# Performance work log

Measured on AMD Instinct MI355X. Metric: run time of the kernel, lower is better.

## Reference

```python
import jax, jax.numpy as jnp
import numpy as np

B, Qn, Kn, QD, KVD, FFN, H = 8, 1024, 2048, 512, 256, 2048, 8


def _layer_norm(x, g, b, eps=1e-5):
    m = jnp.mean(x, axis=-1, keepdims=True)
    v = jnp.mean((x - m) ** 2, axis=-1, keepdims=True)
    return (x - m) * jax.lax.rsqrt(v + eps) * g + b


def _mha(q, k, v, key_padding_mask, num_heads):
    # q,k: [B,S,D], v: [B,K,Dv]; reshape to per-head, scale by sqrt(key head dim)
    b, qn, d = q.shape
    kn = k.shape[1]
    dh = d // num_heads
    q = q.reshape(b, qn, num_heads, dh)
    k = k.reshape(b, kn, num_heads, dh)
    v = v.reshape(b, kn, num_heads, -1)
    attn = jnp.einsum('bqhd,bkhd->bhqk', q, k) / jnp.asarray(np.sqrt(dh), q.dtype)
    attn = jnp.where(key_padding_mask[:, None, None, :], -jnp.inf, attn)
    attn = jax.nn.softmax(attn, axis=-1)
    out = jnp.einsum('bhqk,bkhd->bqhd', attn, v)  # [B,Q,H,dv]
    return out.reshape(b, qn, -1)


def setup_inputs() -> dict:
    key = jax.random.key(0)
    ks = jax.random.split(key, 32)
    s = 0.02
    inp = {
        'queries_data': jax.random.normal(ks[0], (B, Qn, QD), jnp.float32),
        'queries_mask': jnp.zeros((B, Qn), bool),
        'box_pos': jax.random.normal(ks[1], (B, Qn, 4 * KVD), jnp.float32),
        'center_pos': jax.random.normal(ks[2], (B, Qn, 2 * KVD), jnp.float32),
        'kv_data': jax.random.normal(ks[3], (B, Kn, KVD), jnp.float32),
        'kv_mask': jnp.zeros((B, Kn), bool),
        'kv_pos': jax.random.normal(ks[4], (B, Kn, KVD), jnp.float32),
        # params ([in,out] convention)
        'sa_qkv_w': jax.random.normal(ks[5], (QD, 3 * QD), jnp.float32) * s,
        'sa_qkv_b': jnp.zeros((3 * QD,), jnp.float32),
        'sa_pos_w': jax.random.normal(ks[6], (4 * KVD, 2 * QD), jnp.float32) * s,
        'sa_pos_b': jnp.zeros((2 * QD,), jnp.float32),
        'sa_ln_g': jnp.ones((QD,), jnp.float32),
        'sa_ln_b': jnp.zeros((QD,), jnp.float32),
        'ca_q_w': jax.random.normal(ks[7], (QD, QD), jnp.float32) * s,
        'ca_q_b': jnp.zeros((QD,), jnp.float32),
        'ca_kv_w': jax.random.normal(ks[8], (KVD, 2 * QD), jnp.float32) * s,
        'ca_kv_b': jnp.zeros((2 * QD,), jnp.float32),
        'ca_qpos_w': jax.random.normal(ks[9], (2 * KVD, QD), jnp.float32) * s,
        'ca_qpos_b': jnp.zeros((QD,), jnp.float32),
        'ca_kpos_w': jax.random.normal(ks[10], (KVD, QD), jnp.float32) * s,
        'ca_kpos_b': jnp.zeros((QD,), jnp.float32),
        'ca_ln_g': jnp.ones((QD,), jnp.float32),
        'ca_ln_b': jnp.zeros((QD,), jnp.float32),
        'ffn_w1': jax.random.normal(ks[11], (QD, FFN), jnp.float32) * s,
        'ffn_b1': jnp.zeros((FFN,), jnp.float32),
        'ffn_w2': jax.random.normal(ks[12], (FFN, QD), jnp.float32) * s,
        'ffn_b2': jnp.zeros((QD,), jnp.float32),
        'ffn_ln_g': jnp.ones((QD,), jnp.float32),
        'ffn_ln_b': jnp.zeros((QD,), jnp.float32),
    }
    return inp


def reference(queries_data, queries_mask, box_pos, center_pos, kv_data, kv_mask, kv_pos,
              sa_qkv_w, sa_qkv_b, sa_pos_w, sa_pos_b, sa_ln_g, sa_ln_b,
              ca_q_w, ca_q_b, ca_kv_w, ca_kv_b, ca_qpos_w, ca_qpos_b,
              ca_kpos_w, ca_kpos_b, ca_ln_g, ca_ln_b,
              ffn_w1, ffn_b1, ffn_w2, ffn_b2, ffn_ln_g, ffn_ln_b):
    # ---- self-attention (pos added to q,k) ----
    qkv = queries_data @ sa_qkv_w + sa_qkv_b
    q, k, v = jnp.split(qkv, 3, axis=-1)
    q_pos, k_pos = jnp.split(box_pos @ sa_pos_w + sa_pos_b, 2, axis=-1)
    sa_out = _mha(q + q_pos, k + k_pos, v, queries_mask, H)
    sa_out = _layer_norm(queries_data + sa_out, sa_ln_g, sa_ln_b)
    # ---- cross-attention (pos concatenated per head) ----
    q = sa_out @ ca_q_w + ca_q_b
    k, v = jnp.split(kv_data @ ca_kv_w + ca_kv_b, 2, axis=-1)
    q_pos = center_pos @ ca_qpos_w + ca_qpos_b
    k_pos = kv_pos @ ca_kpos_w + ca_kpos_b
    dh = QD // H
    q = jnp.concatenate([q.reshape(B, Qn, H, dh), q_pos.reshape(B, Qn, H, dh)], axis=-1).reshape(B, Qn, -1)
    k = jnp.concatenate([k.reshape(B, Kn, H, dh), k_pos.reshape(B, Kn, H, dh)], axis=-1).reshape(B, Kn, -1)
    ca_out = _mha(q, k, v, kv_mask, H)
    ca_out = _layer_norm(sa_out + ca_out, ca_ln_g, ca_ln_b)
    # ---- FFN ----
    f = jax.nn.relu(ca_out @ ffn_w1 + ffn_b1) @ ffn_w2 + ffn_b2
    return _layer_norm(ca_out + f, ffn_ln_g, ffn_ln_b)
```

## Files before the change

kernel.cpp:

```cpp
#include <hip/hip_runtime.h>

typedef __attribute__((ext_vector_type(4))) float f32x4;
typedef __attribute__((ext_vector_type(8))) short bf16x8;
typedef __attribute__((ext_vector_type(4))) unsigned int u32x4;

static __device__ __forceinline__ short f2bf(float f){
    unsigned int u = __builtin_bit_cast(unsigned int, f);
    unsigned int r = (u + 0x7fffu + ((u >> 16) & 1u)) >> 16;
    return (short)r;
}
static __device__ __forceinline__ void gload_lds16(const void* g, void* l){
    __builtin_amdgcn_global_load_lds((const __attribute__((address_space(1))) void*)g,
                                     (__attribute__((address_space(3))) void*)l, 16, 0, 0);
}
static __device__ __forceinline__ float exp2fast(float x){
    float r; asm("v_exp_f32 %0, %1" : "=v"(r) : "v"(x)); return r;
}
static __device__ __forceinline__ unsigned int packbf(float lo, float hi){
#if __has_builtin(__builtin_amdgcn_perm)
    return __builtin_amdgcn_perm(__builtin_bit_cast(unsigned int, hi),
                                 __builtin_bit_cast(unsigned int, lo), 0x07060302u);
#else
    return (__builtin_bit_cast(unsigned int, hi) & 0xffff0000u) |
           (__builtin_bit_cast(unsigned int, lo) >> 16);
#endif
}
static __device__ __forceinline__ void prio_hi(){
#if defined(__HIP_DEVICE_COMPILE__)
    __builtin_amdgcn_s_setprio(1);
#endif
}
static __device__ __forceinline__ void prio_lo(){
#if defined(__HIP_DEVICE_COMPILE__)
    __builtin_amdgcn_s_setprio(0);
#endif
}

static __device__ __forceinline__ void transcast_body(const float* __restrict__ w,
                                                      short* __restrict__ wT,
                                                      int K, int N, int bx, int by, int t){
    int n = bx * 256 + t;
    int k0 = by * 8;
    bf16x8 o;
#pragma unroll
    for (int j = 0; j < 8; j++) o[j] = f2bf(w[(long)(k0 + j) * N + n]);
    *(bf16x8*)(wT + (long)n * K + k0) = o;
}
__global__ __launch_bounds__(256) void prep_weights(
    const float* __restrict__ queries, const float* __restrict__ box,
    const float* __restrict__ ctr, const float* __restrict__ kvd, const float* __restrict__ kvp,
    const unsigned char* __restrict__ qmask, const unsigned char* __restrict__ kmask,
    const float* __restrict__ b_qkv, const float* __restrict__ b_pos,
    short* __restrict__ Xcat, short* __restrict__ ctr_bf,
    short* __restrict__ kvd_bf, short* __restrict__ kvp_bf,
    float* __restrict__ mb_sa, float* __restrict__ mb_ca, float* __restrict__ bcomb,
    const float* __restrict__ w_qkv, const float* __restrict__ w_pos,
    const float* __restrict__ w_caq, const float* __restrict__ w_cakv,
    const float* __restrict__ w_caqp, const float* __restrict__ w_cakp,
    const float* __restrict__ w_f1, const float* __restrict__ w_f2,
    short* __restrict__ wTm_qk, short* __restrict__ wTv,
    short* __restrict__ wT_caq, short* __restrict__ wT_cakv,
    short* __restrict__ wT_caqp, short* __restrict__ wT_cakp,
    short* __restrict__ wT_f1, short* __restrict__ wT_f2)
{
    int bb = blockIdx.x, t = threadIdx.x;
    if (bb < 12288){
        const float* src; short* dst; long i; long stride; int logRow; int colOff;
        if (bb < 2048){ src = queries; dst = Xcat; i = ((long)bb * 256 + t) * 8; logRow = 9;  stride = 1536; colOff = 0; }
        else if (bb < 6144){ src = box; dst = Xcat; i = ((long)(bb - 2048) * 256 + t) * 8; logRow = 10; stride = 1536; colOff = 512; }
        else if (bb < 8192){ src = ctr; dst = ctr_bf; i = ((long)(bb - 6144) * 256 + t) * 8; logRow = 0; stride = 0; colOff = 0; }
        else if (bb < 10240){ src = kvd; dst = kvd_bf; i = ((long)(bb - 8192) * 256 + t) * 8; logRow = 0; stride = 0; colOff = 0; }
        else { src = kvp; dst = kvp_bf; i = ((long)(bb - 10240) * 256 + t) * 8; logRow = 0; stride = 0; colOff = 0; }
        f32x4 a = *(const f32x4*)(src + i);
        f32x4 b = *(const f32x4*)(src + i + 4);
        bf16x8 o;
#pragma unroll
        for (int j = 0; j < 4; j++){ o[j] = f2bf(a[j]); o[4 + j] = f2bf(b[j]); }
        long oi = logRow ? ((i >> logRow) * stride + colOff + (i & ((1L << logRow) - 1))) : i;
        *(bf16x8*)(dst + oi) = o;
        return;
    }
    if (bb < 12320){ int i = (bb - 12288) * 256 + t; mb_sa[i] = qmask[i] ? -1e30f : 0.f; return; }
    if (bb < 12384){ int i = (bb - 12320) * 256 + t; mb_ca[i] = kmask[i] ? -1e30f : 0.f; return; }
    if (bb < 12388){ int i = (bb - 12384) * 256 + t; if (i < 1024) bcomb[i] = b_qkv[i] + b_pos[i]; return; }
    int wb = bb - 12388;
    if (wb < 768){
        int by = wb / 4, bx = wb % 4;
        int n = bx * 256 + t;
        int k0 = by * 8;
        bf16x8 o;
#pragma unroll
        for (int j = 0; j < 8; j++){
            int kk = k0 + j;
            float v = (kk < 512) ? w_qkv[(long)kk * 1536 + n] : w_pos[(long)(kk - 512) * 1024 + n];
            o[j] = f2bf(v);
        }
        *(bf16x8*)(wTm_qk + (long)n * 1536 + k0) = o;
    }
    else if (wb < 896){
        int lb = wb - 768;
        int by = lb / 2, bx = lb % 2;
        int n = bx * 256 + t;
        int k0 = by * 8;
        bf16x8 o;
#pragma unroll
        for (int j = 0; j < 8; j++) o[j] = f2bf(w_qkv[(long)(k0 + j) * 1536 + 1024 + n]);
        *(bf16x8*)(wTv + (long)n * 512 + k0) = o;
    }
    else if (wb < 1024){ int lb = wb - 896;  transcast_body(w_caq,  wT_caq,  512, 512,  lb % 2, lb / 2, t); }
    else if (wb < 1152){ int lb = wb - 1024; transcast_body(w_cakv, wT_cakv, 256, 1024, lb % 4, lb / 4, t); }
    else if (wb < 1280){ int lb = wb - 1152; transcast_body(w_caqp, wT_caqp, 512, 512,  lb % 2, lb / 2, t); }
    else if (wb < 1344){ int lb = wb - 1280; transcast_body(w_cakp, wT_cakp, 256, 512,  lb % 2, lb / 2, t); }
    else if (wb < 1856){ int lb = wb - 1344; transcast_body(w_f1,   wT_f1,   512, 2048, lb % 8, lb / 8, t); }
    else               { int lb = wb - 1856; transcast_body(w_f2,   wT_f2,   2048, 512, lb % 2, lb / 2, t); }
}

struct GD {
    const short* A; const short* Bt; const float* bias;
    short* Cbf; float* Cf; short* Vt;
    long lda;
    int N, K, flags, vtColBase, snShift, vtSN, blkStart, nbx, nblk;
};
struct GD4 { GD g[4]; int n; };

__global__ __launch_bounds__(128, 3) void gemm_multi(GD4 dd)
{
    constexpr int BN = 64, BLOCK = 128;
    constexpr int BUF = (128 + BN) * 32;
    constexpr int EST = BN + 4;
    __shared__ __attribute__((aligned(16))) char smem[2 * BUF * 2];
    float* lC = (float*)smem;
    int bb = blockIdx.x;
    int si = 0;
#pragma unroll
    for (int i = 1; i < 4; i++) if (i < dd.n && bb >= dd.g[i].blkStart) si = i;
    const short* A = dd.g[si].A;
    const short* Bt = dd.g[si].Bt;
    const float* bias = dd.g[si].bias;
    short* Cbf = dd.g[si].Cbf;
    float* Cf = dd.g[si].Cf;
    short* Vt = dd.g[si].Vt;
    long lda = dd.g[si].lda;
    int N = dd.g[si].N, K = dd.g[si].K, flags = dd.g[si].flags;
    int vtColBase = dd.g[si].vtColBase, snShift = dd.g[si].snShift, vtSN = dd.g[si].vtSN;
    int nbx = dd.g[si].nbx, nblk = dd.g[si].nblk;

    int t = threadIdx.x, w = t >> 6, l = t & 63;
    int cl = l & 15, g = l >> 4;
    int flat = bb - dd.g[si].blkStart;
    int q8 = nblk >> 3;
    int swz = (flat & 7) * q8 + (flat >> 3);
    long r0 = (long)(swz / nbx) * 128, c0 = (long)(swz % nbx) * BN;
    int wr = w;
    f32x4 acc[4][4];
#pragma unroll
    for (int mi = 0; mi < 4; mi++)
#pragma unroll
        for (int ni = 0; ni < 4; ni++) acc[mi][ni] = f32x4{0.f, 0.f, 0.f, 0.f};

    auto stage = [&](int d, int k0){
        char* lA = smem + (size_t)d * BUF * 2;
        char* lB = lA + 128 * 32 * 2;
#pragma unroll
        for (int i = 0; i < 4; i++){
            int s = i * BLOCK + t;
            int row = s >> 2, blk = s & 3;
            int sb = blk ^ (row & 3);
            gload_lds16(A + (r0 + row) * lda + k0 + sb * 8, lA + i * (BLOCK * 16) + w * 1024);
        }
#pragma unroll
        for (int i = 0; i < 2; i++){
            int s = i * BLOCK + t;
            int row = s >> 2, blk = s & 3;
            int sb = blk ^ (row & 3);
            gload_lds16(Bt + (c0 + row) * (long)K + k0 + sb * 8, lB + i * (BLOCK * 16) + w * 1024);
        }
    };

    stage(0, 0);
    __syncthreads();
    int NK = K / 32;
    for (int kt = 0; kt < NK; kt++){
        int cur = kt & 1;
        if (kt + 1 < NK) stage(cur ^ 1, (kt + 1) * 32);
        const short* lA = (const short*)(smem + (size_t)cur * BUF * 2);
        const short* lB = lA + 128 * 32;
        bf16x8 af[4], bfr[4];
#pragma unroll
        for (int mi = 0; mi < 4; mi++){
            int row = wr * 64 + mi * 16 + cl;
            af[mi] = *(const bf16x8*)(lA + row * 32 + (g ^ (row & 3)) * 8);
        }
#pragma unroll
        for (int ni = 0; ni < 4; ni++){
            int row = ni * 16 + cl;
            bfr[ni] = *(const bf16x8*)(lB + row * 32 + (g ^ (row & 3)) * 8);
        }
        prio_hi();
#pragma unroll
        for (int mi = 0; mi < 4; mi++)
#pragma unroll
            for (int ni = 0; ni < 4; ni++)
                acc[mi][ni] = __builtin_amdgcn_mfma_f32_16x16x32_bf16(af[mi], bfr[ni], acc[mi][ni], 0, 0, 0);
        prio_lo();
        __syncthreads();
    }

    bool vtBlock = (flags & 4) && (c0 >= vtColBase);
#pragma unroll
    for (int mi = 0; mi < 4; mi++){
        __syncthreads();
#pragma unroll
        for (int ni = 0; ni < 4; ni++)
#pragma unroll
            for (int rr = 0; rr < 4; rr++)
                lC[(wr * 16 + g * 4 + rr) * EST + ni * 16 + cl] = acc[mi][ni][rr];
        __syncthreads();
        if (vtBlock){
#pragma unroll
            for (int c2 = 0; c2 < 2; c2++){
                int task = t + BLOCK * c2;
                int col = task & 63;
                int wrg = (task >> 6) & 1;
                int ch = task >> 7;
                float bv = bias[c0 + col];
                long qg0 = r0 + wrg * 64 + mi * 16 + ch * 8;
                bf16x8 ob;
#pragma unroll
                for (int j = 0; j < 8; j++)
                    ob[j] = f2bf(lC[(wrg * 16 + ch * 8 + j) * EST + col] + bv);
                long dvg = c0 - vtColBase + col;
                long h = dvg >> 6, dvv = dvg & 63;
                long b = qg0 >> snShift;
                long loc = qg0 & ((1L << snShift) - 1);
                *(bf16x8*)(Vt + ((b * 8 + h) * 64 + dvv) * (long)vtSN + loc) = ob;
            }
        } else {
#pragma unroll
            for (int c2 = 0; c2 < 2; c2++){
                int chunk = t + BLOCK * c2;
                int row = chunk >> 3;
                int coloff = (chunk & 7) * 8;
                long grow = r0 + (row >> 4) * 64 + mi * 16 + (row & 15);
                long gcol = c0 + coloff;
                f32x4 bv0 = *(const f32x4*)(bias + gcol);
                f32x4 bv1 = *(const f32x4*)(bias + gcol + 4);
                float v[8];
#pragma unroll
                for (int j = 0; j < 8; j++){
                    float x = lC[row * EST + coloff + j] + (j < 4 ? bv0[j] : bv1[j - 4]);
                    if (flags & 1) x = fmaxf(x, 0.f);
                    v[j] = x;
                }
                if (Cf){
                    *(f32x4*)(Cf + grow * N + gcol) = f32x4{v[0], v[1], v[2], v[3]};
                    *(f32x4*)(Cf + grow * N + gcol + 4) = f32x4{v[4], v[5], v[6], v[7]};
                } else {
                    bf16x8 ob;
#pragma unroll
                    for (int j = 0; j < 8; j++) ob[j] = f2bf(v[j]);
                    long idx;
                    if (flags & 2){
                        long part = gcol >> 9;
                        long cc = gcol & 511;
                        long b = grow >> 10, qn = grow & 1023;
                        long h = cc >> 6, d = cc & 63;
                        idx = ((part * 64 + b * 8 + h) * 1024 + qn) * 64 + d;
                    } else if (flags & 4){
                        idx = grow * (long)vtColBase + gcol;
                    } else {
                        idx = grow * N + gcol;
                    }
                    *(bf16x8*)(Cbf + idx) = ob;
                }
            }
        }
    }
}

__global__ __launch_bounds__(256) void ln_fuse(const float* __restrict__ a, const float* __restrict__ b,
                                               const float* __restrict__ g, const float* __restrict__ be,
                                               float* __restrict__ outf, short* __restrict__ outb){
    int w = threadIdx.x >> 6, l = threadIdx.x & 63;
    long row = (long)blockIdx.x * 4 + w;
    long base = row * 512 + l * 8;
    f32x4 a0 = *(const f32x4*)(a + base);
    f32x4 a1 = *(const f32x4*)(a + base + 4);
    f32x4 b0 = *(const f32x4*)(b + base);
    f32x4 b1 = *(const f32x4*)(b + base + 4);
    float x[8]; float s = 0.f, s2 = 0.f;
#pragma unroll
    for (int j = 0; j < 4; j++){ x[j] = a0[j] + b0[j]; x[4 + j] = a1[j] + b1[j]; }
#pragma unroll
    for (int j = 0; j < 8; j++){ s += x[j]; s2 += x[j] * x[j]; }
#pragma unroll
    for (int o = 1; o < 64; o <<= 1){ s += __shfl_xor(s, o); s2 += __shfl_xor(s2, o); }
    float mean = s * (1.f / 512.f);
    float rstd = rsqrtf(s2 * (1.f / 512.f) - mean * mean + 1e-5f);
    int c = l * 8;
    f32x4 y0, y1; bf16x8 ob;
#pragma unroll
    for (int j = 0; j < 4; j++){
        float y = (x[j] - mean) * rstd * g[c + j] + be[c + j];
        y0[j] = y; ob[j] = f2bf(y);
    }
#pragma unroll
    for (int j = 0; j < 4; j++){
        float y = (x[4 + j] - mean) * rstd * g[c + 4 + j] + be[c + 4 + j];
        y1[j] = y; ob[4 + j] = f2bf(y);
    }
    *(f32x4*)(outf + base) = y0;
    *(f32x4*)(outf + base + 4) = y1;
    if (outb) *(bf16x8*)(outb + base) = ob;
}

template<int DH, int KN, bool CAT>
__global__ __launch_bounds__(256, 2) void attn_kernel(
    const short* __restrict__ Q1, const short* __restrict__ Q2,
    const short* __restrict__ K1, const short* __restrict__ K2,
    const short* __restrict__ Vt,
    const float* __restrict__ mbias, float* __restrict__ out, float scale2)
{
    constexpr int KT = 64, DV = 64, Qn = 1024, H = 8;
    constexpr int NF = DH / 32;
    constexpr int BPR = DH / 8;
    constexpr int KITER = KT * BPR / 256;
    constexpr int NT = KN / KT;
    __shared__ __attribute__((aligned(16))) short lK[2][KT * DH];
    __shared__ __attribute__((aligned(16))) short lV[2][DV * KT];
    int t = threadIdx.x, w = t >> 6, l = t & 63;
    int cl = l & 15, g = l >> 4;
    int bid = blockIdx.x;
    int bh = (bid & 7) * 8 + (bid >> 6);
    int qb = (bid >> 3) & 7;
    int b = bh >> 3, h = bh & 7;
    int q0 = qb * 128 + w * 32;

    bf16x8 qf[2][NF];
#pragma unroll
    for (int qq = 0; qq < 2; qq++)
#pragma unroll
        for (int f = 0; f < NF; f++){
            if constexpr (CAT){
                const short* src = (f < NF / 2) ? Q1 : Q2;
                qf[qq][f] = *(const bf16x8*)(src + ((long)b * Qn + q0 + qq * 16 + cl) * 512 + h * 64
                                             + (f & (NF / 2 - 1)) * 32 + 8 * g);
            } else {
                qf[qq][f] = *(const bf16x8*)(Q1 + ((long)bh * Qn + q0 + qq * 16 + cl) * DH + f * 32 + 8 * g);
            }
        }

    const short* kp[KITER];
    long kstep[KITER];
#pragma unroll
    for (int i = 0; i < KITER; i++){
        int s_ = i * 256 + t;
        int srow_ = s_ / BPR, blk = s_ % BPR;
        int s32 = srow_ & 31;
        int key = (srow_ & 32) + 8 * ((s32 >> 2) & 3) + 4 * (s32 >> 4) + (s32 & 3);
        int sb = blk ^ (srow_ & 7);
        if constexpr (CAT){
            if (sb < 8){ kp[i] = K1 + ((long)b * KN + key) * 512 + h * 64 + sb * 8; kstep[i] = (long)KT * 512; }
            else       { kp[i] = K2 + ((long)b * KN + key) * 512 + h * 64 + (sb - 8) * 8; kstep[i] = (long)KT * 512; }
        } else {
            kp[i] = K1 + ((long)bh * KN + key) * DH + sb * 8; kstep[i] = (long)KT * DH;
        }
    }
    const short* vp[2];
#pragma unroll
    for (int i = 0; i < 2; i++){
        int s_ = i * 256 + t;
        int srow_ = s_ >> 3, blk = s_ & 7;
        int sb = blk ^ (srow_ & 7);
        vp[i] = Vt + ((long)bh * DV + srow_) * KN + sb * 8;
    }

    auto stage = [&](int d){
#pragma unroll
        for (int i = 0; i < KITER; i++){
            gload_lds16(kp[i], (char*)(&lK[d][0]) + i * 4096 + w * 1024);
            kp[i] += kstep[i];
        }
#pragma unroll
        for (int i = 0; i < 2; i++){
            gload_lds16(vp[i], (char*)(&lV[d][0]) + i * 4096 + w * 1024);
            vp[i] += KT;
        }
    };

    f32x4 st[2][4];
    auto do_qk = [&](int d){
        prio_hi();
#pragma unroll
        for (int o = 0; o < 4; o++){
            int srow_ = o * 16 + cl;
            bf16x8 kf[NF];
#pragma unroll
            for (int f = 0; f < NF; f++){
                int sb = (4 * f + g) ^ (srow_ & 7);
                kf[f] = *(const bf16x8*)(&lK[d][0] + srow_ * DH + sb * 8);
            }
#pragma unroll
            for (int qq = 0; qq < 2; qq++){
                f32x4 acc = f32x4{0.f, 0.f, 0.f, 0.f};
#pragma unroll
                for (int f = 0; f < NF; f++)
                    acc = __builtin_amdgcn_mfma_f32_16x16x32_bf16(kf[f], qf[qq][f], acc, 0, 0, 0);
                st[qq][o] = acc;
            }
        }
        prio_lo();
    };

    const float* mrow = mbias + (long)b * KN;
    bf16x8 vones;
    {
        u32x4 ou; ou[0] = ou[1] = ou[2] = ou[3] = 0x3F803F80u;
        vones = __builtin_bit_cast(bf16x8, ou);
    }
    f32x4 lacc[2];
    f32x4 oacc[2][4];
#pragma unroll
    for (int qq = 0; qq < 2; qq++){
        lacc[qq] = f32x4{0.f, 0.f, 0.f, 0.f};
#pragma unroll
        for (int d = 0; d < 4; d++) oacc[qq][d] = f32x4{0.f, 0.f, 0.f, 0.f};
    }

    f32x4 mb[4];
#pragma unroll
    for (int o = 0; o < 4; o++)
        mb[o] = *(const f32x4*)(mrow + (o >> 1) * 32 + 8 * g + 4 * (o & 1));

    stage(0);
    __syncthreads();
    do_qk(0);

    for (int tt = 0; tt < NT; tt++){
        int cur = tt & 1;
        if (tt + 1 < NT) stage(cur ^ 1);

        bf16x8 pa[2][2];
#pragma unroll
        for (int qq = 0; qq < 2; qq++){
#pragma unroll
            for (int kb = 0; kb < 2; kb++){
                float pA[4], pB[4];
#pragma unroll
                for (int rr = 0; rr < 4; rr++){
                    pA[rr] = exp2fast(fmaf(st[qq][2 * kb][rr], scale2, mb[2 * kb][rr]));
                    pB[rr] = exp2fast(fmaf(st[qq][2 * kb + 1][rr], scale2, mb[2 * kb + 1][rr]));
                }
                u32x4 pk;
                pk[0] = packbf(pA[0], pA[1]);
                pk[1] = packbf(pA[2], pA[3]);
                pk[2] = packbf(pB[0], pB[1]);
                pk[3] = packbf(pB[2], pB[3]);
                pa[qq][kb] = __builtin_bit_cast(bf16x8, pk);
            }
        }
        if (tt + 1 < NT){
#pragma unroll
            for (int o = 0; o < 4; o++)
                mb[o] = *(const f32x4*)(mrow + (tt + 1) * KT + (o >> 1) * 32 + 8 * g + 4 * (o & 1));
        }
        prio_hi();
#pragma unroll
        for (int qq = 0; qq < 2; qq++){
            lacc[qq] = __builtin_amdgcn_mfma_f32_16x16x32_bf16(pa[qq][0], vones, lacc[qq], 0, 0, 0);
            lacc[qq] = __builtin_amdgcn_mfma_f32_16x16x32_bf16(pa[qq][1], vones, lacc[qq], 0, 0, 0);
        }
#pragma unroll
        for (int dvc = 0; dvc < 4; dvc++){
            int vrow = dvc * 16 + cl;
            bf16x8 vf[2];
#pragma unroll
            for (int kb = 0; kb < 2; kb++){
                int sb = (4 * kb + g) ^ (vrow & 7);
                vf[kb] = *(const bf16x8*)(&lV[cur][0] + vrow * KT + sb * 8);
            }
#pragma unroll
            for (int qq = 0; qq < 2; qq++){
                f32x4 o = oacc[qq][dvc];
                o = __builtin_amdgcn_mfma_f32_16x16x32_bf16(pa[qq][0], vf[0], o, 0, 0, 0);
                o = __builtin_amdgcn_mfma_f32_16x16x32_bf16(pa[qq][1], vf[1], o, 0, 0, 0);
                oacc[qq][dvc] = o;
            }
        }
        prio_lo();
        __syncthreads();
        if (tt + 1 < NT) do_qk(cur ^ 1);
    }

#pragma unroll
    for (int qq = 0; qq < 2; qq++){
        float linv[4];
#pragma unroll
        for (int rr = 0; rr < 4; rr++) linv[rr] = 1.f / lacc[qq][rr];
#pragma unroll
        for (int dvc = 0; dvc < 4; dvc++)
#pragma unroll
            for (int rr = 0; rr < 4; rr++){
                int q = q0 + qq * 16 + 4 * g + rr;
                out[(((long)b * Qn + q) * H + h) * DV + dvc * 16 + cl] = oacc[qq][dvc][rr] * linv[rr];
            }
    }
}

extern "C" void kernel_launch(void* const* d_in, const int* in_sizes, int n_in,
                              void* d_out, int out_size, void* d_ws, size_t ws_size,
                              hipStream_t stream)
{
    (void)in_sizes; (void)n_in; (void)out_size; (void)ws_size;
    const int Qn = 1024, Kn = 2048;
    const long MQ = 8L * Qn;
    const long MK = 8L * Kn;

    const float* queries = (const float*)d_in[0];
    const unsigned char* qmask = (const unsigned char*)d_in[1];
    const float* box  = (const float*)d_in[2];
    const float* ctr  = (const float*)d_in[3];
    const float* kvd  = (const float*)d_in[4];
    const unsigned char* kmask = (const unsigned char*)d_in[5];
    const float* kvp  = (const float*)d_in[6];
    const float* w_qkv = (const float*)d_in[7];  const float* b_qkv = (const float*)d_in[8];
    const float* w_pos = (const float*)d_in[9];  const float* b_pos = (const float*)d_in[10];
    const float* g_sa  = (const float*)d_in[11]; const float* be_sa = (const float*)d_in[12];
    const float* w_caq = (const float*)d_in[13]; const float* b_caq = (const float*)d_in[14];
    const float* w_cakv = (const float*)d_in[15]; const float* b_cakv = (const float*)d_in[16];
    const float* w_caqp = (const float*)d_in[17]; const float* b_caqp = (const float*)d_in[18];
    const float* w_cakp = (const float*)d_in[19]; const float* b_cakp = (const float*)d_in[20];
    const float* g_ca  = (const float*)d_in[21]; const float* be_ca = (const float*)d_in[22];
    const float* w_f1  = (const float*)d_in[23]; const float* b_f1 = (const float*)d_in[24];
    const float* w_f2  = (const float*)d_in[25]; const float* b_f2 = (const float*)d_in[26];
    const float* g_f   = (const float*)d_in[27]; const float* be_f = (const float*)d_in[28];

    char* ws = (char*)d_ws;
    size_t off = 0;
    auto alloc = [&](size_t bytes) -> char* {
        char* p = ws + off;
        off += (bytes + 255) & ~(size_t)255;
        return p;
    };
    short* wTm_qk  = (short*)alloc(1024L * 1536 * 2);
    short* wTv     = (short*)alloc(512L * 512 * 2);
    short* wT_caq  = (short*)alloc(512L * 512 * 2);
    short* wT_cakv = (short*)alloc(1024L * 256 * 2);
    short* wT_caqp = (short*)alloc(512L * 512 * 2);
    short* wT_cakp = (short*)alloc(512L * 256 * 2);
    short* wT_f1   = (short*)alloc(2048L * 512 * 2);
    short* wT_f2   = (short*)alloc(512L * 2048 * 2);
    float* bcomb   = (float*)alloc(1024L * 4);
    short* ctr_bf  = (short*)alloc(MQ * 512 * 2);
    short* kvd_bf  = (short*)alloc(MK * 256 * 2);
    short* kvp_bf  = (short*)alloc(MK * 256 * 2);
    short* saln_bf = (short*)alloc(MQ * 512 * 2);
    short* caln_bf = (short*)alloc(MQ * 512 * 2);
    float* sa_ln_f = (float*)alloc(MQ * 512 * 4);
    float* ca_ln_f = (float*)alloc(MQ * 512 * 4);
    float* att_f   = (float*)alloc(MQ * 512 * 4);
    float* f_out   = (float*)alloc(MQ * 512 * 4);
    short* VtSA    = (short*)alloc(64L * 64 * 1024 * 2);
    short* VtCA    = (short*)alloc(64L * 64 * 2048 * 2);
    float* mb_sa   = (float*)alloc(MQ * 4);
    float* mb_ca   = (float*)alloc(MK * 4);
    char* zone1 = alloc(MK * 1024 * 2);
    char* zone2 = alloc(MQ * 2048 * 2);
    char* zone3 = alloc(MK * 512 * 2);
    char* zone4 = alloc(MQ * 512 * 2);
    char* zone5 = alloc(MQ * 512 * 2);

    auto mkgd = [&](const short* A, long lda, const short* Bt, const float* bias,
                    short* Cbf, float* Cf, int M, int N, int K, int flags,
                    short* Vt, int vtColBase, int snShift, int vtSN, int blkStart) -> GD {
        GD d;
        d.A = A; d.Bt = Bt; d.bias = bias; d.Cbf = Cbf; d.Cf = Cf; d.Vt = Vt;
        d.lda = lda; d.N = N; d.K = K; d.flags = flags;
        d.vtColBase = vtColBase; d.snShift = snShift; d.vtSN = vtSN;
        d.blkStart = blkStart; d.nbx = N / 64; d.nblk = (N / 64) * (M / 128);
        return d;
    };
    auto launch_multi = [&](GD4& dd){
        int total = 0;
        for (int i = 0; i < dd.n; i++) total += dd.g[i].nblk;
        for (int i = dd.n; i < 4; i++){ dd.g[i] = dd.g[0]; dd.g[i].blkStart = 0x7fffffff; }
        gemm_multi<<<dim3(total), dim3(128), 0, stream>>>(dd);
    };

    short* Xcat = (short*)zone1;
    prep_weights<<<dim3(14756), dim3(256), 0, stream>>>(
        queries, box, ctr, kvd, kvp, qmask, kmask, b_qkv, b_pos,
        Xcat, ctr_bf, kvd_bf, kvp_bf, mb_sa, mb_ca, bcomb,
        w_qkv, w_pos, w_caq, w_cakv, w_caqp, w_cakp, w_f1, w_f2,
        wTm_qk, wTv, wT_caq, wT_cakv, wT_caqp, wT_cakp, wT_f1, wT_f2);

    short* QKVa = (short*)zone2;
    short* Qa  = QKVa;
    short* Ka  = QKVa + 64L * 1024 * 64;
    {
        GD4 dd; dd.n = 2;
        dd.g[0] = mkgd(Xcat, 1536, wTm_qk, bcomb, QKVa, nullptr, (int)MQ, 1024, 1536, 2,
                       nullptr, 0, 0, 0, 0);
        dd.g[1] = mkgd(Xcat, 1536, wTv, b_qkv + 1024, nullptr, nullptr, (int)MQ, 512, 512, 4,
                       VtSA, 0, 10, 1024, dd.g[0].nblk);
        launch_multi(dd);
    }

    attn_kernel<64, 1024, false><<<dim3(512), dim3(256), 0, stream>>>(
        Qa, nullptr, Ka, nullptr, VtSA, mb_sa, att_f, 0.125f * 1.44269504f);

    ln_fuse<<<dim3((unsigned)(MQ / 4)), dim3(256), 0, stream>>>(queries, att_f, g_sa, be_sa, sa_ln_f, saln_bf);

    short* caq_bf  = (short*)zone4;
    short* caqp_bf = (short*)zone5;
    short* caK     = (short*)zone1;
    short* cakp_bf = (short*)zone3;
    {
        GD4 dd; dd.n = 4;
        int s0 = 0;
        dd.g[0] = mkgd(kvd_bf, 256, wT_cakv, b_cakv, caK, nullptr, (int)MK, 1024, 256, 4,
                       VtCA, 512, 11, 2048, s0);                    s0 += dd.g[0].nblk;
        dd.g[1] = mkgd(kvp_bf, 256, wT_cakp, b_cakp, cakp_bf, nullptr, (int)MK, 512, 256, 0,
                       nullptr, 0, 0, 0, s0);                       s0 += dd.g[1].nblk;
        dd.g[2] = mkgd(saln_bf, 512, wT_caq, b_caq, caq_bf, nullptr, (int)MQ, 512, 512, 0,
                       nullptr, 0, 0, 0, s0);                       s0 += dd.g[2].nblk;
        dd.g[3] = mkgd(ctr_bf, 512, wT_caqp, b_caqp, caqp_bf, nullptr, (int)MQ, 512, 512, 0,
                       nullptr, 0, 0, 0, s0);
        launch_multi(dd);
    }

    attn_kernel<128, 2048, true><<<dim3(512), dim3(256), 0, stream>>>(
        caq_bf, caqp_bf, caK, cakp_bf, VtCA, mb_ca, att_f, 0.08838834764831845f * 1.44269504f);

    ln_fuse<<<dim3((unsigned)(MQ / 4)), dim3(256), 0, stream>>>(sa_ln_f, att_f, g_ca, be_ca, ca_ln_f, caln_bf);

    short* mid_bf = (short*)zone2;
    {
        GD4 dd; dd.n = 1;
        dd.g[0] = mkgd(caln_bf, 512, wT_f1, b_f1, mid_bf, nullptr, (int)MQ, 2048, 512, 1,
                       nullptr, 0, 0, 0, 0);
        launch_multi(dd);
    }
    {
        GD4 dd; dd.n = 1;
        dd.g[0] = mkgd(mid_bf, 2048, wT_f2, b_f2, nullptr, f_out, (int)MQ, 512, 2048, 0,
                       nullptr, 0, 0, 0, 0);
        launch_multi(dd);
    }

    ln_fuse<<<dim3((unsigned)(MQ / 4)), dim3(256), 0, stream>>>(ca_ln_f, f_out, g_f, be_f, (float*)d_out, (short*)nullptr);
}
```

Measured before the change: 317.9 us.

## Triple-buffer GEMM K-loop and batch independent cross-attention projections earlier

The GEMM main loop moves from double to triple buffering. Raw barriers with explicit vmcnt waits let two stages of global-to-LDS loads stay in flight, which should hide memory latency better. The cross-attention K/V, k-pos and q-pos projections do not depend on self-attention, so they move into the first grouped GEMM launch, leaving only the Q projection after self-attention LN. In exchange, LDS per block grows and occupancy drops from 3 to 2 blocks per CU, and the buffers that used to share memory zones now get dedicated allocations.

```diff
diff --git a/kernel.cpp b/kernel.cpp
--- a/kernel.cpp
+++ b/kernel.cpp
@@ -33,6 +33,11 @@
 static __device__ __forceinline__ void prio_lo(){
 #if defined(__HIP_DEVICE_COMPILE__)
     __builtin_amdgcn_s_setprio(0);
+#endif
+}
+static __device__ __forceinline__ void barrier_raw(){
+#if defined(__HIP_DEVICE_COMPILE__)
+    __builtin_amdgcn_s_barrier();
 #endif
 }
 
@@ -121,19 +126,19 @@
     long lda;
     int N, K, flags, vtColBase, snShift, vtSN, blkStart, nbx, nblk;
 };
-struct GD4 { GD g[4]; int n; };
-
-__global__ __launch_bounds__(128, 3) void gemm_multi(GD4 dd)
+struct GD6 { GD g[6]; int n; };
+
+__global__ __launch_bounds__(128, 2) void gemm_multi(GD6 dd)
 {
     constexpr int BN = 64, BLOCK = 128;
     constexpr int BUF = (128 + BN) * 32;
     constexpr int EST = BN + 4;
-    __shared__ __attribute__((aligned(16))) char smem[2 * BUF * 2];
+    __shared__ __attribute__((aligned(16))) char smem[3 * BUF * 2];
     float* lC = (float*)smem;
     int bb = blockIdx.x;
     int si = 0;
 #pragma unroll
-    for (int i = 1; i < 4; i++) if (i < dd.n && bb >= dd.g[i].blkStart) si = i;
+    for (int i = 1; i < 6; i++) if (i < dd.n && bb >= dd.g[i].blkStart) si = i;
     const short* A = dd.g[si].A;
     const short* Bt = dd.g[si].Bt;
     const float* bias = dd.g[si].bias;
@@ -177,13 +182,22 @@
         }
     };
 
+    int NK = K / 32;
     stage(0, 0);
-    __syncthreads();
-    int NK = K / 32;
+    stage(1, 32);
+    int bc = 0, bs = 2;
     for (int kt = 0; kt < NK; kt++){
-        int cur = kt & 1;
-        if (kt + 1 < NK) stage(cur ^ 1, (kt + 1) * 32);
-        const short* lA = (const short*)(smem + (size_t)cur * BUF * 2);
+        if (kt + 2 < NK){
+            stage(bs, (kt + 2) * 32);
+            bs = (bs == 2) ? 0 : bs + 1;
+            asm volatile("s_waitcnt vmcnt(12)" ::: "memory");
+        } else if (kt + 1 < NK){
+            asm volatile("s_waitcnt vmcnt(6)" ::: "memory");
+        } else {
+            asm volatile("s_waitcnt vmcnt(0)" ::: "memory");
+        }
+        barrier_raw();
+        const short* lA = (const short*)(smem + (size_t)bc * BUF * 2);
         const short* lB = lA + 128 * 32;
         bf16x8 af[4], bfr[4];
 #pragma unroll
@@ -203,7 +217,9 @@
             for (int ni = 0; ni < 4; ni++)
                 acc[mi][ni] = __builtin_amdgcn_mfma_f32_16x16x32_bf16(af[mi], bfr[ni], acc[mi][ni], 0, 0, 0);
         prio_lo();
-        __syncthreads();
+        asm volatile("s_waitcnt lgkmcnt(0)" ::: "memory");
+        barrier_raw();
+        bc = (bc == 2) ? 0 : bc + 1;
     }
 
     bool vtBlock = (flags & 4) && (c0 >= vtColBase);
@@ -564,11 +580,12 @@
     short* VtCA    = (short*)alloc(64L * 64 * 2048 * 2);
     float* mb_sa   = (float*)alloc(MQ * 4);
     float* mb_ca   = (float*)alloc(MK * 4);
-    char* zone1 = alloc(MK * 1024 * 2);
+    short* caK     = (short*)alloc(MK * 512 * 2);
+    short* cakp_bf = (short*)alloc(MK * 512 * 2);
+    short* caq_bf  = (short*)alloc(MQ * 512 * 2);
+    short* caqp_bf = (short*)alloc(MQ * 512 * 2);
+    char* zone1 = alloc(MQ * 1536 * 2);
     char* zone2 = alloc(MQ * 2048 * 2);
-    char* zone3 = alloc(MK * 512 * 2);
-    char* zone4 = alloc(MQ * 512 * 2);
-    char* zone5 = alloc(MQ * 512 * 2);
 
     auto mkgd = [&](const short* A, long lda, const short* Bt, const float* bias,
                     short* Cbf, float* Cf, int M, int N, int K, int flags,
@@ -580,10 +597,10 @@
         d.blkStart = blkStart; d.nbx = N / 64; d.nblk = (N / 64) * (M / 128);
         return d;
     };
-    auto launch_multi = [&](GD4& dd){
+    auto launch_multi = [&](GD6& dd){
         int total = 0;
         for (int i = 0; i < dd.n; i++) total += dd.g[i].nblk;
-        for (int i = dd.n; i < 4; i++){ dd.g[i] = dd.g[0]; dd.g[i].blkStart = 0x7fffffff; }
+        for (int i = dd.n; i < 6; i++){ dd.g[i] = dd.g[0]; dd.g[i].blkStart = 0x7fffffff; }
         gemm_multi<<<dim3(total), dim3(128), 0, stream>>>(dd);
     };
 
@@ -598,11 +615,18 @@
     short* Qa  = QKVa;
     short* Ka  = QKVa + 64L * 1024 * 64;
     {
-        GD4 dd; dd.n = 2;
+        GD6 dd; dd.n = 5;
+        int s0 = 0;
         dd.g[0] = mkgd(Xcat, 1536, wTm_qk, bcomb, QKVa, nullptr, (int)MQ, 1024, 1536, 2,
-                       nullptr, 0, 0, 0, 0);
-        dd.g[1] = mkgd(Xcat, 1536, wTv, b_qkv + 1024, nullptr, nullptr, (int)MQ, 512, 512, 4,
-                       VtSA, 0, 10, 1024, dd.g[0].nblk);
+                       nullptr, 0, 0, 0, s0);                       s0 += dd.g[0].nblk;
+        dd.g[1] = mkgd(kvd_bf, 256, wT_cakv, b_cakv, caK, nullptr, (int)MK, 1024, 256, 4,
+                       VtCA, 512, 11, 2048, s0);                    s0 += dd.g[1].nblk;
+        dd.g[2] = mkgd(kvp_bf, 256, wT_cakp, b_cakp, cakp_bf, nullptr, (int)MK, 512, 256, 0,
+                       nullptr, 0, 0, 0, s0);                       s0 += dd.g[2].nblk;
+        dd.g[3] = mkgd(Xcat, 1536, wTv, b_qkv + 1024, nullptr, nullptr, (int)MQ, 512, 512, 4,
+                       VtSA, 0, 10, 1024, s0);                      s0 += dd.g[3].nblk;
+        dd.g[4] = mkgd(ctr_bf, 512, wT_caqp, b_caqp, caqp_bf, nullptr, (int)MQ, 512, 512, 0,
+                       nullptr, 0, 0, 0, s0);
         launch_multi(dd);
     }
 
@@ -611,21 +635,10 @@
 
     ln_fuse<<<dim3((unsigned)(MQ / 4)), dim3(256), 0, stream>>>(queries, att_f, g_sa, be_sa, sa_ln_f, saln_bf);
 
-    short* caq_bf  = (short*)zone4;
-    short* caqp_bf = (short*)zone5;
-    short* caK     = (short*)zone1;
-    short* cakp_bf = (short*)zone3;
     {
-        GD4 dd; dd.n = 4;
-        int s0 = 0;
-        dd.g[0] = mkgd(kvd_bf, 256, wT_cakv, b_cakv, caK, nullptr, (int)MK, 1024, 256, 4,
-                       VtCA, 512, 11, 2048, s0);                    s0 += dd.g[0].nblk;
-        dd.g[1] = mkgd(kvp_bf, 256, wT_cakp, b_cakp, cakp_bf, nullptr, (int)MK, 512, 256, 0,
-                       nullptr, 0, 0, 0, s0);                       s0 += dd.g[1].nblk;
-        dd.g[2] = mkgd(saln_bf, 512, wT_caq, b_caq, caq_bf, nullptr, (int)MQ, 512, 512, 0,
-                       nullptr, 0, 0, 0, s0);                       s0 += dd.g[2].nblk;
-        dd.g[3] = mkgd(ctr_bf, 512, wT_caqp, b_caqp, caqp_bf, nullptr, (int)MQ, 512, 512, 0,
-                       nullptr, 0, 0, 0, s0);
+        GD6 dd; dd.n = 1;
+        dd.g[0] = mkgd(saln_bf, 512, wT_caq, b_caq, caq_bf, nullptr, (int)MQ, 512, 512, 0,
+                       nullptr, 0, 0, 0, 0);
         launch_multi(dd);
     }
 
@@ -636,13 +649,13 @@
 
     short* mid_bf = (short*)zone2;
     {
-        GD4 dd; dd.n = 1;
+        GD6 dd; dd.n = 1;
         dd.g[0] = mkgd(caln_bf, 512, wT_f1, b_f1, mid_bf, nullptr, (int)MQ, 2048, 512, 1,
                        nullptr, 0, 0, 0, 0);
         launch_multi(dd);
     }
     {
-        GD4 dd; dd.n = 1;
+        GD6 dd; dd.n = 1;
         dd.g[0] = mkgd(mid_bf, 2048, wT_f2, b_f2, nullptr, f_out, (int)MQ, 512, 2048, 0,
                        nullptr, 0, 0, 0, 0);
         launch_multi(dd);
```

New measurement: 319.6 us. Within noise of the previous version (+0.5%).
